# Kernel optimization log

Measured on AMD Instinct MI355X. Metric: run time of the kernel, lower is better.

The kernel has to match this reference:

```python
import jax, jax.numpy as jnp
import numpy as np

DIM = 256
WINDOW = 8
NUM_HEADS = 8
N = WINDOW * WINDOW  # tokens per window
HEAD_DIM = DIM // NUM_HEADS
SCALE = HEAD_DIM ** -0.5
B_ = 2048


def _relative_position_index(w):
    coords = np.stack(np.meshgrid(np.arange(w), np.arange(w), indexing='ij'))  # 2,w,w
    cf = coords.reshape(2, -1)  # 2,N
    rel = cf[:, :, None] - cf[:, None, :]  # 2,N,N
    rel = rel.transpose(1, 2, 0) + (w - 1)  # N,N,2 in [0, 2w-2]
    return rel[..., 0] * (2 * w - 1) + rel[..., 1]  # N,N

REL_INDEX = jnp.asarray(_relative_position_index(WINDOW))  # (N,N) int


def setup_inputs() -> dict:
    key = jax.random.key(0)
    ks = jax.random.split(key, 8)
    x = jax.random.normal(ks[0], (B_, N, DIM), dtype=jnp.float32)
    mask = jax.random.normal(ks[1], (B_, 1, N, N), dtype=jnp.float32)
    w_qkv = jax.random.normal(ks[2], (3 * DIM, DIM), dtype=jnp.float32) * (DIM ** -0.5)
    b_qkv = jnp.zeros((3 * DIM,), dtype=jnp.float32)
    w_proj = jax.random.normal(ks[3], (DIM, DIM), dtype=jnp.float32) * (DIM ** -0.5)
    b_proj = jnp.zeros((DIM,), dtype=jnp.float32)
    bias_table = jax.random.normal(ks[4], ((2 * WINDOW - 1) ** 2, NUM_HEADS), dtype=jnp.float32) * 0.02
    return {"x": x, "mask": mask, "w_qkv": w_qkv, "b_qkv": b_qkv,
            "w_proj": w_proj, "b_proj": b_proj, "bias_table": bias_table}


def reference(x, mask, w_qkv, b_qkv, w_proj, b_proj, bias_table):
    Bw, n, c = x.shape
    qkv = x @ w_qkv.T + b_qkv  # (B_, N, 3*C)
    qkv = qkv.reshape(Bw, n, 3, NUM_HEADS, HEAD_DIM)
    q = qkv[:, :, 0].transpose(0, 2, 1, 3) * SCALE  # (B_, H, N, hd)
    k = qkv[:, :, 1].transpose(0, 2, 1, 3)
    v = qkv[:, :, 2].transpose(0, 2, 1, 3)
    attn = jnp.einsum('bhnd,bhmd->bhnm', q, k)  # (B_, H, N, N)
    rel_bias = bias_table[REL_INDEX]  # (N, N, H)
    attn = attn + rel_bias.transpose(2, 0, 1)[None]  # broadcast (1,H,N,N)
    attn = attn + mask  # (B_,1,N,N) broadcasts over heads
    attn = jax.nn.softmax(attn, axis=-1)
    out = jnp.einsum('bhnm,bhmd->bhnd', attn, v)  # (B_, H, N, hd)
    out = out.transpose(0, 2, 1, 3).reshape(Bw, n, c)
    return out @ w_proj.T + b_proj
```

## Files before the change

kernel.cpp:

```cpp
#include <hip/hip_runtime.h>

#define NWIN 2048
#define NTOK 64
#define CDIM 256
#define NH 8
#define HD 32
#define QSCALE 0.17677669529663689f

#define LDA 264
#define LDQ 36
#define LDV 72
#define LDP 68

typedef __bf16 bf16x4 __attribute__((ext_vector_type(4)));
typedef __bf16 bf16x8 __attribute__((ext_vector_type(8)));
typedef float  f32x4  __attribute__((ext_vector_type(4)));

__device__ __forceinline__ unsigned short f2bf(float f) {
    union { float f; unsigned u; } v; v.f = f;
    unsigned r = v.u + 0x7FFFu + ((v.u >> 16) & 1u);
    return (unsigned short)(r >> 16);
}

__device__ __forceinline__ bf16x8 ld16(const unsigned short* p) {
    return *(const bf16x8*)p;
}
__device__ __forceinline__ bf16x8 ld8u(const unsigned short* p) {
    bf16x4 lo = *(const bf16x4*)p;
    bf16x4 hi = *(const bf16x4*)(p + 4);
    return __builtin_shufflevector(lo, hi, 0, 1, 2, 3, 4, 5, 6, 7);
}

__global__ void precast_kernel(const float* __restrict__ wq, const float* __restrict__ wp,
                               const float* __restrict__ bt,
                               unsigned short* __restrict__ wqb, unsigned short* __restrict__ wpb,
                               float* __restrict__ relbT) {
    int i = blockIdx.x * 256 + threadIdx.x;
    if (i < 196608) {
        wqb[i] = f2bf(wq[i]);
    } else if (i < 262144) {
        wpb[i - 196608] = f2bf(wp[i - 196608]);
    } else if (i < 294912) {
        int j = i - 262144;
        int h = j >> 12;
        int c = (j >> 6) & 63;
        int r = j & 63;
        int yi = r >> 3, xi = r & 7, yj = c >> 3, xj = c & 7;
        int idx = (yi - yj + 7) * 15 + (xi - xj + 7);
        relbT[j] = bt[idx * NH + h];
    }
}

__global__ __launch_bounds__(512, 2)
void win_attn_kernel(const float* __restrict__ x, const float* __restrict__ mask,
                     const float* __restrict__ bq, const float* __restrict__ bp,
                     const unsigned short* __restrict__ wq, const unsigned short* __restrict__ wp,
                     const float* __restrict__ relbT, float* __restrict__ out) {
    __shared__ __align__(16) unsigned short sm[80896];
    unsigned short* sA = sm;
    unsigned short* sQ = sm + 16896;
    unsigned short* sK = sm + 35328;
    unsigned short* sV = sm + 53760;
    unsigned short* sP = sm + 72192;

    const int b    = blockIdx.x;
    const int tid  = threadIdx.x;
    const int wv   = tid >> 6;
    const int lane = tid & 63;
    const int lm   = lane & 15;
    const int quad = lane >> 4;
    const f32x4 fzero = {0.f, 0.f, 0.f, 0.f};

    {
        const int row = tid >> 3;
        const int c0  = (tid & 7) * 32;
        const float4* gx = (const float4*)(x + ((size_t)b * NTOK + row) * CDIM + c0);
        unsigned short* dst = sA + row * LDA + c0;
        #pragma unroll
        for (int i = 0; i < 8; ++i) {
            float4 v = gx[i];
            ushort4 u;
            u.x = f2bf(v.x); u.y = f2bf(v.y); u.z = f2bf(v.z); u.w = f2bf(v.w);
            *(ushort4*)(dst + i * 4) = u;
        }
    }
    __syncthreads();

    {
        const int h = wv;
        const int nbase[6] = { h*HD, h*HD + 16,
                               CDIM + h*HD, CDIM + h*HD + 16,
                               2*CDIM + h*HD, 2*CDIM + h*HD + 16 };
        f32x4 acc[4][6];
        #pragma unroll
        for (int mt = 0; mt < 4; ++mt)
            #pragma unroll
            for (int t = 0; t < 6; ++t) acc[mt][t] = fzero;

        #pragma unroll
        for (int ks = 0; ks < 8; ++ks) {
            bf16x8 bfr[6];
            #pragma unroll
            for (int t = 0; t < 6; ++t)
                bfr[t] = ld16(wq + (nbase[t] + lm) * CDIM + ks * 32 + quad * 8);
            bf16x8 afr[4];
            #pragma unroll
            for (int mt = 0; mt < 4; ++mt)
                afr[mt] = ld16(sA + (mt * 16 + lm) * LDA + ks * 32 + quad * 8);
            #pragma unroll
            for (int mt = 0; mt < 4; ++mt)
                #pragma unroll
                for (int t = 0; t < 6; ++t)
                    acc[mt][t] = __builtin_amdgcn_mfma_f32_16x16x32_bf16(afr[mt], bfr[t], acc[mt][t], 0, 0, 0);
        }

        float bqv[6];
        #pragma unroll
        for (int t = 0; t < 6; ++t) bqv[t] = bq[nbase[t] + lm];

        unsigned short* sQh = sQ + h * (NTOK * LDQ);
        unsigned short* sKh = sK + h * (NTOK * LDQ);
        unsigned short* sVh = sV + h * (HD * LDV);
        #pragma unroll
        for (int mt = 0; mt < 4; ++mt) {
            #pragma unroll
            for (int t = 0; t < 6; ++t) {
                #pragma unroll
                for (int reg = 0; reg < 4; ++reg) {
                    float val = acc[mt][t][reg] + bqv[t];
                    int tok = mt * 16 + quad * 4 + reg;
                    if (t < 2)      sQh[tok * LDQ + t * 16 + lm]          = f2bf(val * QSCALE);
                    else if (t < 4) sKh[tok * LDQ + (t - 2) * 16 + lm]    = f2bf(val);
                    else            sVh[((t - 4) * 16 + lm) * LDV + tok]  = f2bf(val);
                }
            }
        }
    }
    __syncthreads();

    {
        const int h = wv;
        const unsigned short* sQh = sQ + h * (NTOK * LDQ);
        const unsigned short* sKh = sK + h * (NTOK * LDQ);
        const unsigned short* sVh = sV + h * (HD * LDV);
        unsigned short* sPh = sP + wv * (16 * LDP);

        bf16x8 kf[4];
        #pragma unroll
        for (int jt = 0; jt < 4; ++jt)
            kf[jt] = ld8u(sKh + (jt * 16 + lm) * LDQ + quad * 8);
        bf16x8 vf[2][2];
        #pragma unroll
        for (int nt = 0; nt < 2; ++nt)
            #pragma unroll
            for (int kk = 0; kk < 2; ++kk)
                vf[nt][kk] = ld16(sVh + (nt * 16 + lm) * LDV + kk * 32 + quad * 8);

        const float* maskb = mask + (size_t)b * (NTOK * NTOK);
        const float* relh  = relbT + h * (NTOK * NTOK);

        for (int rc = 0; rc < 4; ++rc) {
            const int m0 = rc * 16;
            bf16x8 qa = ld8u(sQh + (m0 + lm) * LDQ + quad * 8);
            f32x4 s[4];
            #pragma unroll
            for (int jt = 0; jt < 4; ++jt)
                s[jt] = __builtin_amdgcn_mfma_f32_16x16x32_bf16(qa, kf[jt], fzero, 0, 0, 0);

            #pragma unroll
            for (int jt = 0; jt < 4; ++jt) {
                float4 rb4 = *(const float4*)(relh + (jt * 16 + lm) * 64 + m0 + quad * 4);
                float rbv[4] = { rb4.x, rb4.y, rb4.z, rb4.w };
                #pragma unroll
                for (int reg = 0; reg < 4; ++reg) {
                    int r = m0 + quad * 4 + reg;
                    s[jt][reg] += rbv[reg] + maskb[r * 64 + jt * 16 + lm];
                }
            }

            float mx[4], inv[4];
            #pragma unroll
            for (int reg = 0; reg < 4; ++reg) {
                float m_ = fmaxf(fmaxf(s[0][reg], s[1][reg]), fmaxf(s[2][reg], s[3][reg]));
                #pragma unroll
                for (int off = 1; off < 16; off <<= 1)
                    m_ = fmaxf(m_, __shfl_xor(m_, off, 64));
                mx[reg] = m_;
            }
            float p[4][4];
            #pragma unroll
            for (int jt = 0; jt < 4; ++jt)
                #pragma unroll
                for (int reg = 0; reg < 4; ++reg)
                    p[jt][reg] = __expf(s[jt][reg] - mx[reg]);
            #pragma unroll
            for (int reg = 0; reg < 4; ++reg) {
                float s_ = (p[0][reg] + p[1][reg]) + (p[2][reg] + p[3][reg]);
                #pragma unroll
                for (int off = 1; off < 16; off <<= 1)
                    s_ += __shfl_xor(s_, off, 64);
                inv[reg] = 1.0f / s_;
            }

            #pragma unroll
            for (int jt = 0; jt < 4; ++jt)
                #pragma unroll
                for (int reg = 0; reg < 4; ++reg)
                    sPh[(quad * 4 + reg) * LDP + jt * 16 + lm] = f2bf(p[jt][reg]);

            bf16x8 pa0 = ld8u(sPh + lm * LDP + quad * 8);
            bf16x8 pa1 = ld8u(sPh + lm * LDP + 32 + quad * 8);
            #pragma unroll
            for (int nt = 0; nt < 2; ++nt) {
                f32x4 o = __builtin_amdgcn_mfma_f32_16x16x32_bf16(pa0, vf[nt][0], fzero, 0, 0, 0);
                o = __builtin_amdgcn_mfma_f32_16x16x32_bf16(pa1, vf[nt][1], o, 0, 0, 0);
                #pragma unroll
                for (int reg = 0; reg < 4; ++reg) {
                    int r = m0 + quad * 4 + reg;
                    sA[r * LDA + h * HD + nt * 16 + lm] = f2bf(o[reg] * inv[reg]);
                }
            }
        }
    }
    __syncthreads();

    {
        const int n0 = wv * HD;
        f32x4 acc[4][2];
        #pragma unroll
        for (int mt = 0; mt < 4; ++mt) { acc[mt][0] = fzero; acc[mt][1] = fzero; }

        #pragma unroll
        for (int ks = 0; ks < 8; ++ks) {
            bf16x8 bfr[2];
            #pragma unroll
            for (int nt = 0; nt < 2; ++nt)
                bfr[nt] = ld16(wp + (n0 + nt * 16 + lm) * CDIM + ks * 32 + quad * 8);
            bf16x8 afr[4];
            #pragma unroll
            for (int mt = 0; mt < 4; ++mt)
                afr[mt] = ld16(sA + (mt * 16 + lm) * LDA + ks * 32 + quad * 8);
            #pragma unroll
            for (int mt = 0; mt < 4; ++mt)
                #pragma unroll
                for (int nt = 0; nt < 2; ++nt)
                    acc[mt][nt] = __builtin_amdgcn_mfma_f32_16x16x32_bf16(afr[mt], bfr[nt], acc[mt][nt], 0, 0, 0);
        }

        float bpv[2] = { bp[n0 + lm], bp[n0 + 16 + lm] };
        #pragma unroll
        for (int mt = 0; mt < 4; ++mt)
            #pragma unroll
            for (int nt = 0; nt < 2; ++nt)
                #pragma unroll
                for (int reg = 0; reg < 4; ++reg) {
                    int r = mt * 16 + quad * 4 + reg;
                    out[((size_t)b * NTOK + r) * CDIM + n0 + nt * 16 + lm] = acc[mt][nt][reg] + bpv[nt];
                }
    }
}

extern "C" void kernel_launch(void* const* d_in, const int* in_sizes, int n_in,
                              void* d_out, int out_size, void* d_ws, size_t ws_size,
                              hipStream_t stream) {
    const float* x    = (const float*)d_in[0];
    const float* mask = (const float*)d_in[1];
    const float* wq   = (const float*)d_in[2];
    const float* bq   = (const float*)d_in[3];
    const float* wp   = (const float*)d_in[4];
    const float* bp   = (const float*)d_in[5];
    const float* bt   = (const float*)d_in[6];

    unsigned short* wqb   = (unsigned short*)d_ws;
    unsigned short* wpb   = wqb + 196608;
    float*          relbT = (float*)((char*)d_ws + 524288);
    float*          out   = (float*)d_out;

    precast_kernel<<<1152, 256, 0, stream>>>(wq, wp, bt, wqb, wpb, relbT);
    win_attn_kernel<<<NWIN, 512, 0, stream>>>(x, mask, bq, bp, wqb, wpb, relbT, out);
}
```

Before: 435.5 us.

## Split projection into separate kernel and shrink LDS in attention kernel

The fused kernel is split in two. The attention kernel now uses 256 threads, each wave handling two heads in sequence, and a small per-wave scratch buffer laid out in MFMA-fragment order. That cuts LDS use from about 160KB to 48KB per block so more blocks can be resident. It also prefetches mask rows one chunk ahead and uses a fast reciprocal. The attention output goes as bf16 into the output buffer, and a new projection kernel reads it back per window and overwrites it in place with the fp32 result. This adds a global write and read of the intermediate, and the Q, K and V GEMMs are now computed separately per head.

```diff
diff --git a/kernel.cpp b/kernel.cpp
--- a/kernel.cpp
+++ b/kernel.cpp
@@ -7,28 +7,17 @@
 #define HD 32
 #define QSCALE 0.17677669529663689f
 
-#define LDA 264
-#define LDQ 36
-#define LDV 72
-#define LDP 68
-
-typedef __bf16 bf16x4 __attribute__((ext_vector_type(4)));
 typedef __bf16 bf16x8 __attribute__((ext_vector_type(8)));
 typedef float  f32x4  __attribute__((ext_vector_type(4)));
+typedef unsigned short u16x8 __attribute__((ext_vector_type(8)));
 
 __device__ __forceinline__ unsigned short f2bf(float f) {
     union { float f; unsigned u; } v; v.f = f;
     unsigned r = v.u + 0x7FFFu + ((v.u >> 16) & 1u);
     return (unsigned short)(r >> 16);
 }
-
 __device__ __forceinline__ bf16x8 ld16(const unsigned short* p) {
     return *(const bf16x8*)p;
-}
-__device__ __forceinline__ bf16x8 ld8u(const unsigned short* p) {
-    bf16x4 lo = *(const bf16x4*)p;
-    bf16x4 hi = *(const bf16x4*)(p + 4);
-    return __builtin_shufflevector(lo, hi, 0, 1, 2, 3, 4, 5, 6, 7);
 }
 
 __global__ void precast_kernel(const float* __restrict__ wq, const float* __restrict__ wp,
@@ -51,17 +40,225 @@
     }
 }
 
-__global__ __launch_bounds__(512, 2)
+__global__ __launch_bounds__(256, 3)
 void win_attn_kernel(const float* __restrict__ x, const float* __restrict__ mask,
-                     const float* __restrict__ bq, const float* __restrict__ bp,
-                     const unsigned short* __restrict__ wq, const unsigned short* __restrict__ wp,
-                     const float* __restrict__ relbT, float* __restrict__ out) {
-    __shared__ __align__(16) unsigned short sm[80896];
-    unsigned short* sA = sm;
-    unsigned short* sQ = sm + 16896;
-    unsigned short* sK = sm + 35328;
-    unsigned short* sV = sm + 53760;
-    unsigned short* sP = sm + 72192;
+                     const float* __restrict__ bqkv,
+                     const unsigned short* __restrict__ wq,
+                     const float* __restrict__ relbT,
+                     unsigned short* __restrict__ aout) {
+    __shared__ __align__(16) unsigned short sm[24576];
+
+    const int b    = blockIdx.x;
+    const int tid  = threadIdx.x;
+    const int wv   = tid >> 6;
+    const int lane = tid & 63;
+    const int lm   = lane & 15;
+    const int quad = lane >> 4;
+    unsigned short* scr = sm + 16384 + wv * 2048;
+    const f32x4 fzero = {0.f, 0.f, 0.f, 0.f};
+
+    {
+        const int row = tid >> 2;
+        const int mt = row >> 4, lr = row & 15;
+        const float* gx = x + ((size_t)b * NTOK + row) * CDIM;
+        #pragma unroll
+        for (int kk = 0; kk < 2; ++kk) {
+            const int ks = (tid & 3) * 2 + kk;
+            #pragma unroll
+            for (int q = 0; q < 4; ++q) {
+                float4 v0 = *(const float4*)(gx + ks * 32 + q * 8);
+                float4 v1 = *(const float4*)(gx + ks * 32 + q * 8 + 4);
+                u16x8 u;
+                u[0] = f2bf(v0.x); u[1] = f2bf(v0.y); u[2] = f2bf(v0.z); u[3] = f2bf(v0.w);
+                u[4] = f2bf(v1.x); u[5] = f2bf(v1.y); u[6] = f2bf(v1.z); u[7] = f2bf(v1.w);
+                *(u16x8*)(sm + (mt * 8 + ks) * 512 + (lr + 16 * q) * 8) = u;
+            }
+        }
+    }
+    __syncthreads();
+
+    const float* maskb = mask + (size_t)b * (NTOK * NTOK);
+
+    for (int hi = 0; hi < 2; ++hi) {
+        const int h = wv + hi * 4;
+
+        const float bq0 = bqkv[h * HD + lm],            bq1 = bqkv[h * HD + 16 + lm];
+        const float bk0 = bqkv[CDIM + h * HD + lm],     bk1 = bqkv[CDIM + h * HD + 16 + lm];
+        const float bv0 = bqkv[2 * CDIM + h * HD + lm], bv1 = bqkv[2 * CDIM + h * HD + 16 + lm];
+
+        f32x4 aq[2][4], ak[2][4];
+        #pragma unroll
+        for (int t = 0; t < 2; ++t)
+            #pragma unroll
+            for (int mt = 0; mt < 4; ++mt) { aq[t][mt] = fzero; ak[t][mt] = fzero; }
+
+        #pragma unroll
+        for (int ks = 0; ks < 8; ++ks) {
+            bf16x8 bfq0 = ld16(wq + ((h * HD + lm) * CDIM) + ks * 32 + quad * 8);
+            bf16x8 bfq1 = ld16(wq + ((h * HD + 16 + lm) * CDIM) + ks * 32 + quad * 8);
+            bf16x8 bfk0 = ld16(wq + ((CDIM + h * HD + lm) * CDIM) + ks * 32 + quad * 8);
+            bf16x8 bfk1 = ld16(wq + ((CDIM + h * HD + 16 + lm) * CDIM) + ks * 32 + quad * 8);
+            #pragma unroll
+            for (int mt = 0; mt < 4; ++mt) {
+                bf16x8 afr = ld16(sm + (mt * 8 + ks) * 512 + lane * 8);
+                aq[0][mt] = __builtin_amdgcn_mfma_f32_16x16x32_bf16(afr, bfq0, aq[0][mt], 0, 0, 0);
+                aq[1][mt] = __builtin_amdgcn_mfma_f32_16x16x32_bf16(afr, bfq1, aq[1][mt], 0, 0, 0);
+                ak[0][mt] = __builtin_amdgcn_mfma_f32_16x16x32_bf16(afr, bfk0, ak[0][mt], 0, 0, 0);
+                ak[1][mt] = __builtin_amdgcn_mfma_f32_16x16x32_bf16(afr, bfk1, ak[1][mt], 0, 0, 0);
+            }
+        }
+
+        #pragma unroll
+        for (int mt = 0; mt < 4; ++mt)
+            #pragma unroll
+            for (int kt = 0; kt < 2; ++kt)
+                #pragma unroll
+                for (int reg = 0; reg < 4; ++reg) {
+                    float val = ak[kt][mt][reg] + (kt ? bk1 : bk0);
+                    int lp = quad * 4 + reg + 16 * (kt * 2 + (lm >> 3));
+                    scr[mt * 512 + lp * 8 + (lm & 7)] = f2bf(val);
+                }
+        bf16x8 kf[4];
+        #pragma unroll
+        for (int jt = 0; jt < 4; ++jt) kf[jt] = ld16(scr + jt * 512 + lane * 8);
+
+        #pragma unroll
+        for (int mt = 0; mt < 4; ++mt)
+            #pragma unroll
+            for (int qt = 0; qt < 2; ++qt)
+                #pragma unroll
+                for (int reg = 0; reg < 4; ++reg) {
+                    float val = (aq[qt][mt][reg] + (qt ? bq1 : bq0)) * QSCALE;
+                    int lp = quad * 4 + reg + 16 * (qt * 2 + (lm >> 3));
+                    scr[mt * 512 + lp * 8 + (lm & 7)] = f2bf(val);
+                }
+        bf16x8 qa[4];
+        #pragma unroll
+        for (int mt = 0; mt < 4; ++mt) qa[mt] = ld16(scr + mt * 512 + lane * 8);
+
+        f32x4 av[2][4];
+        #pragma unroll
+        for (int t = 0; t < 2; ++t)
+            #pragma unroll
+            for (int mt = 0; mt < 4; ++mt) av[t][mt] = fzero;
+        #pragma unroll
+        for (int ks = 0; ks < 8; ++ks) {
+            bf16x8 bfv0 = ld16(wq + ((2 * CDIM + h * HD + lm) * CDIM) + ks * 32 + quad * 8);
+            bf16x8 bfv1 = ld16(wq + ((2 * CDIM + h * HD + 16 + lm) * CDIM) + ks * 32 + quad * 8);
+            #pragma unroll
+            for (int mt = 0; mt < 4; ++mt) {
+                bf16x8 afr = ld16(sm + (mt * 8 + ks) * 512 + lane * 8);
+                av[0][mt] = __builtin_amdgcn_mfma_f32_16x16x32_bf16(afr, bfv0, av[0][mt], 0, 0, 0);
+                av[1][mt] = __builtin_amdgcn_mfma_f32_16x16x32_bf16(afr, bfv1, av[1][mt], 0, 0, 0);
+            }
+        }
+
+        #pragma unroll
+        for (int mt = 0; mt < 4; ++mt)
+            #pragma unroll
+            for (int vt = 0; vt < 2; ++vt)
+                #pragma unroll
+                for (int reg = 0; reg < 4; ++reg) {
+                    float val = av[vt][mt][reg] + (vt ? bv1 : bv0);
+                    int tk = quad * 4 + reg;
+                    int lp = lm + 16 * ((mt & 1) * 2 + (tk >> 3));
+                    scr[(vt * 2 + (mt >> 1)) * 512 + lp * 8 + (tk & 7)] = f2bf(val);
+                }
+        bf16x8 vf[2][2];
+        #pragma unroll
+        for (int vt = 0; vt < 2; ++vt)
+            #pragma unroll
+            for (int kk = 0; kk < 2; ++kk)
+                vf[vt][kk] = ld16(scr + (vt * 2 + kk) * 512 + lane * 8);
+
+        const float* relh = relbT + h * (NTOK * NTOK);
+        unsigned short* ao = aout + (size_t)b * (2 * NTOK * CDIM) + h * HD;
+
+        float mnxt[16];
+        #pragma unroll
+        for (int jt = 0; jt < 4; ++jt)
+            #pragma unroll
+            for (int reg = 0; reg < 4; ++reg)
+                mnxt[jt * 4 + reg] = maskb[(quad * 4 + reg) * 64 + jt * 16 + lm];
+
+        #pragma unroll
+        for (int rc = 0; rc < 4; ++rc) {
+            const int m0 = rc * 16;
+            float mcur[16];
+            #pragma unroll
+            for (int i = 0; i < 16; ++i) mcur[i] = mnxt[i];
+            if (rc < 3) {
+                #pragma unroll
+                for (int jt = 0; jt < 4; ++jt)
+                    #pragma unroll
+                    for (int reg = 0; reg < 4; ++reg)
+                        mnxt[jt * 4 + reg] = maskb[(m0 + 16 + quad * 4 + reg) * 64 + jt * 16 + lm];
+            }
+
+            float4 rb[4];
+            #pragma unroll
+            for (int jt = 0; jt < 4; ++jt)
+                rb[jt] = *(const float4*)(relh + (jt * 16 + lm) * 64 + m0 + quad * 4);
+
+            f32x4 s[4];
+            #pragma unroll
+            for (int jt = 0; jt < 4; ++jt)
+                s[jt] = __builtin_amdgcn_mfma_f32_16x16x32_bf16(qa[rc], kf[jt], fzero, 0, 0, 0);
+
+            #pragma unroll
+            for (int jt = 0; jt < 4; ++jt) {
+                float rbv[4] = { rb[jt].x, rb[jt].y, rb[jt].z, rb[jt].w };
+                #pragma unroll
+                for (int reg = 0; reg < 4; ++reg)
+                    s[jt][reg] += rbv[reg] + mcur[jt * 4 + reg];
+            }
+
+            float inv[4];
+            float p[4][4];
+            #pragma unroll
+            for (int reg = 0; reg < 4; ++reg) {
+                float m_ = fmaxf(fmaxf(s[0][reg], s[1][reg]), fmaxf(s[2][reg], s[3][reg]));
+                #pragma unroll
+                for (int off = 1; off < 16; off <<= 1)
+                    m_ = fmaxf(m_, __shfl_xor(m_, off, 64));
+                #pragma unroll
+                for (int jt = 0; jt < 4; ++jt)
+                    p[jt][reg] = __expf(s[jt][reg] - m_);
+                float s_ = (p[0][reg] + p[1][reg]) + (p[2][reg] + p[3][reg]);
+                #pragma unroll
+                for (int off = 1; off < 16; off <<= 1)
+                    s_ += __shfl_xor(s_, off, 64);
+                inv[reg] = __builtin_amdgcn_rcpf(s_);
+            }
+
+            #pragma unroll
+            for (int jt = 0; jt < 4; ++jt)
+                #pragma unroll
+                for (int reg = 0; reg < 4; ++reg) {
+                    int lp = quad * 4 + reg + 16 * ((jt & 1) * 2 + (lm >> 3));
+                    scr[(jt >> 1) * 512 + lp * 8 + (lm & 7)] = f2bf(p[jt][reg]);
+                }
+            bf16x8 pa0 = ld16(scr + lane * 8);
+            bf16x8 pa1 = ld16(scr + 512 + lane * 8);
+
+            #pragma unroll
+            for (int nt = 0; nt < 2; ++nt) {
+                f32x4 o = __builtin_amdgcn_mfma_f32_16x16x32_bf16(pa0, vf[nt][0], fzero, 0, 0, 0);
+                o = __builtin_amdgcn_mfma_f32_16x16x32_bf16(pa1, vf[nt][1], o, 0, 0, 0);
+                #pragma unroll
+                for (int reg = 0; reg < 4; ++reg) {
+                    int r = m0 + quad * 4 + reg;
+                    ao[(size_t)r * CDIM + nt * 16 + lm] = f2bf(o[reg] * inv[reg]);
+                }
+            }
+        }
+    }
+}
+
+__global__ __launch_bounds__(256, 4)
+void proj_kernel(const unsigned short* __restrict__ wp, const float* __restrict__ bp,
+                 float* out) {
+    __shared__ __align__(16) unsigned short sa[16896];
 
     const int b    = blockIdx.x;
     const int tid  = threadIdx.x;
@@ -71,193 +268,55 @@
     const int quad = lane >> 4;
     const f32x4 fzero = {0.f, 0.f, 0.f, 0.f};
 
+    const unsigned short* src = (const unsigned short*)out + (size_t)b * (2 * NTOK * CDIM);
     {
-        const int row = tid >> 3;
-        const int c0  = (tid & 7) * 32;
-        const float4* gx = (const float4*)(x + ((size_t)b * NTOK + row) * CDIM + c0);
-        unsigned short* dst = sA + row * LDA + c0;
+        const int col = (tid & 31) * 8;
         #pragma unroll
         for (int i = 0; i < 8; ++i) {
-            float4 v = gx[i];
-            ushort4 u;
-            u.x = f2bf(v.x); u.y = f2bf(v.y); u.z = f2bf(v.z); u.w = f2bf(v.w);
-            *(ushort4*)(dst + i * 4) = u;
+            const int row = i * 8 + (tid >> 5);
+            bf16x8 v = *(const bf16x8*)(src + row * CDIM + col);
+            *(bf16x8*)(sa + row * 264 + col) = v;
         }
     }
     __syncthreads();
 
-    {
-        const int h = wv;
-        const int nbase[6] = { h*HD, h*HD + 16,
-                               CDIM + h*HD, CDIM + h*HD + 16,
-                               2*CDIM + h*HD, 2*CDIM + h*HD + 16 };
-        f32x4 acc[4][6];
-        #pragma unroll
-        for (int mt = 0; mt < 4; ++mt)
-            #pragma unroll
-            for (int t = 0; t < 6; ++t) acc[mt][t] = fzero;
-
-        #pragma unroll
-        for (int ks = 0; ks < 8; ++ks) {
-            bf16x8 bfr[6];
-            #pragma unroll
-            for (int t = 0; t < 6; ++t)
-                bfr[t] = ld16(wq + (nbase[t] + lm) * CDIM + ks * 32 + quad * 8);
-            bf16x8 afr[4];
-            #pragma unroll
-            for (int mt = 0; mt < 4; ++mt)
-                afr[mt] = ld16(sA + (mt * 16 + lm) * LDA + ks * 32 + quad * 8);
-            #pragma unroll
-            for (int mt = 0; mt < 4; ++mt)
-                #pragma unroll
-                for (int t = 0; t < 6; ++t)
-                    acc[mt][t] = __builtin_amdgcn_mfma_f32_16x16x32_bf16(afr[mt], bfr[t], acc[mt][t], 0, 0, 0);
-        }
-
-        float bqv[6];
-        #pragma unroll
-        for (int t = 0; t < 6; ++t) bqv[t] = bq[nbase[t] + lm];
-
-        unsigned short* sQh = sQ + h * (NTOK * LDQ);
-        unsigned short* sKh = sK + h * (NTOK * LDQ);
-        unsigned short* sVh = sV + h * (HD * LDV);
-        #pragma unroll
-        for (int mt = 0; mt < 4; ++mt) {
-            #pragma unroll
-            for (int t = 0; t < 6; ++t) {
-                #pragma unroll
-                for (int reg = 0; reg < 4; ++reg) {
-                    float val = acc[mt][t][reg] + bqv[t];
-                    int tok = mt * 16 + quad * 4 + reg;
-                    if (t < 2)      sQh[tok * LDQ + t * 16 + lm]          = f2bf(val * QSCALE);
-                    else if (t < 4) sKh[tok * LDQ + (t - 2) * 16 + lm]    = f2bf(val);
-                    else            sVh[((t - 4) * 16 + lm) * LDV + tok]  = f2bf(val);
-                }
-            }
-        }
-    }
-    __syncthreads();
-
-    {
-        const int h = wv;
-        const unsigned short* sQh = sQ + h * (NTOK * LDQ);
-        const unsigned short* sKh = sK + h * (NTOK * LDQ);
-        const unsigned short* sVh = sV + h * (HD * LDV);
-        unsigned short* sPh = sP + wv * (16 * LDP);
-
-        bf16x8 kf[4];
-        #pragma unroll
-        for (int jt = 0; jt < 4; ++jt)
-            kf[jt] = ld8u(sKh + (jt * 16 + lm) * LDQ + quad * 8);
-        bf16x8 vf[2][2];
-        #pragma unroll
-        for (int nt = 0; nt < 2; ++nt)
-            #pragma unroll
-            for (int kk = 0; kk < 2; ++kk)
-                vf[nt][kk] = ld16(sVh + (nt * 16 + lm) * LDV + kk * 32 + quad * 8);
-
-        const float* maskb = mask + (size_t)b * (NTOK * NTOK);
-        const float* relh  = relbT + h * (NTOK * NTOK);
-
-        for (int rc = 0; rc < 4; ++rc) {
-            const int m0 = rc * 16;
-            bf16x8 qa = ld8u(sQh + (m0 + lm) * LDQ + quad * 8);
-            f32x4 s[4];
-            #pragma unroll
-            for (int jt = 0; jt < 4; ++jt)
-                s[jt] = __builtin_amdgcn_mfma_f32_16x16x32_bf16(qa, kf[jt], fzero, 0, 0, 0);
-
-            #pragma unroll
-            for (int jt = 0; jt < 4; ++jt) {
-                float4 rb4 = *(const float4*)(relh + (jt * 16 + lm) * 64 + m0 + quad * 4);
-                float rbv[4] = { rb4.x, rb4.y, rb4.z, rb4.w };
-                #pragma unroll
-                for (int reg = 0; reg < 4; ++reg) {
-                    int r = m0 + quad * 4 + reg;
-                    s[jt][reg] += rbv[reg] + maskb[r * 64 + jt * 16 + lm];
-                }
-            }
-
-            float mx[4], inv[4];
+    const int n0 = wv * 64;
+    f32x4 acc[4][4];
+    #pragma unroll
+    for (int mt = 0; mt < 4; ++mt)
+        #pragma unroll
+        for (int nt = 0; nt < 4; ++nt) acc[mt][nt] = fzero;
+
+    #pragma unroll
+    for (int ks = 0; ks < 8; ++ks) {
+        bf16x8 bfr[4];
+        #pragma unroll
+        for (int nt = 0; nt < 4; ++nt)
+            bfr[nt] = ld16(wp + (n0 + nt * 16 + lm) * CDIM + ks * 32 + quad * 8);
+        bf16x8 afr[4];
+        #pragma unroll
+        for (int mt = 0; mt < 4; ++mt)
+            afr[mt] = ld16(sa + (mt * 16 + lm) * 264 + ks * 32 + quad * 8);
+        #pragma unroll
+        for (int mt = 0; mt < 4; ++mt)
+            #pragma unroll
+            for (int nt = 0; nt < 4; ++nt)
+                acc[mt][nt] = __builtin_amdgcn_mfma_f32_16x16x32_bf16(afr[mt], bfr[nt], acc[mt][nt], 0, 0, 0);
+    }
+
+    float bpv[4];
+    #pragma unroll
+    for (int nt = 0; nt < 4; ++nt) bpv[nt] = bp[n0 + nt * 16 + lm];
+
+    #pragma unroll
+    for (int mt = 0; mt < 4; ++mt)
+        #pragma unroll
+        for (int nt = 0; nt < 4; ++nt)
             #pragma unroll
             for (int reg = 0; reg < 4; ++reg) {
-                float m_ = fmaxf(fmaxf(s[0][reg], s[1][reg]), fmaxf(s[2][reg], s[3][reg]));
-                #pragma unroll
-                for (int off = 1; off < 16; off <<= 1)
-                    m_ = fmaxf(m_, __shfl_xor(m_, off, 64));
-                mx[reg] = m_;
-            }
-            float p[4][4];
-            #pragma unroll
-            for (int jt = 0; jt < 4; ++jt)
-                #pragma unroll
-                for (int reg = 0; reg < 4; ++reg)
-                    p[jt][reg] = __expf(s[jt][reg] - mx[reg]);
-            #pragma unroll
-            for (int reg = 0; reg < 4; ++reg) {
-                float s_ = (p[0][reg] + p[1][reg]) + (p[2][reg] + p[3][reg]);
-                #pragma unroll
-                for (int off = 1; off < 16; off <<= 1)
-                    s_ += __shfl_xor(s_, off, 64);
-                inv[reg] = 1.0f / s_;
-            }
-
-            #pragma unroll
-            for (int jt = 0; jt < 4; ++jt)
-                #pragma unroll
-                for (int reg = 0; reg < 4; ++reg)
-                    sPh[(quad * 4 + reg) * LDP + jt * 16 + lm] = f2bf(p[jt][reg]);
-
-            bf16x8 pa0 = ld8u(sPh + lm * LDP + quad * 8);
-            bf16x8 pa1 = ld8u(sPh + lm * LDP + 32 + quad * 8);
-            #pragma unroll
-            for (int nt = 0; nt < 2; ++nt) {
-                f32x4 o = __builtin_amdgcn_mfma_f32_16x16x32_bf16(pa0, vf[nt][0], fzero, 0, 0, 0);
-                o = __builtin_amdgcn_mfma_f32_16x16x32_bf16(pa1, vf[nt][1], o, 0, 0, 0);
-                #pragma unroll
-                for (int reg = 0; reg < 4; ++reg) {
-                    int r = m0 + quad * 4 + reg;
-                    sA[r * LDA + h * HD + nt * 16 + lm] = f2bf(o[reg] * inv[reg]);
-                }
-            }
-        }
-    }
-    __syncthreads();
-
-    {
-        const int n0 = wv * HD;
-        f32x4 acc[4][2];
-        #pragma unroll
-        for (int mt = 0; mt < 4; ++mt) { acc[mt][0] = fzero; acc[mt][1] = fzero; }
-
-        #pragma unroll
-        for (int ks = 0; ks < 8; ++ks) {
-            bf16x8 bfr[2];
-            #pragma unroll
-            for (int nt = 0; nt < 2; ++nt)
-                bfr[nt] = ld16(wp + (n0 + nt * 16 + lm) * CDIM + ks * 32 + quad * 8);
-            bf16x8 afr[4];
-            #pragma unroll
-            for (int mt = 0; mt < 4; ++mt)
-                afr[mt] = ld16(sA + (mt * 16 + lm) * LDA + ks * 32 + quad * 8);
-            #pragma unroll
-            for (int mt = 0; mt < 4; ++mt)
-                #pragma unroll
-                for (int nt = 0; nt < 2; ++nt)
-                    acc[mt][nt] = __builtin_amdgcn_mfma_f32_16x16x32_bf16(afr[mt], bfr[nt], acc[mt][nt], 0, 0, 0);
-        }
-
-        float bpv[2] = { bp[n0 + lm], bp[n0 + 16 + lm] };
-        #pragma unroll
-        for (int mt = 0; mt < 4; ++mt)
-            #pragma unroll
-            for (int nt = 0; nt < 2; ++nt)
-                #pragma unroll
-                for (int reg = 0; reg < 4; ++reg) {
-                    int r = mt * 16 + quad * 4 + reg;
-                    out[((size_t)b * NTOK + r) * CDIM + n0 + nt * 16 + lm] = acc[mt][nt][reg] + bpv[nt];
-                }
-    }
+                int r = mt * 16 + quad * 4 + reg;
+                out[((size_t)b * NTOK + r) * CDIM + n0 + nt * 16 + lm] = acc[mt][nt][reg] + bpv[nt];
+            }
 }
 
 extern "C" void kernel_launch(void* const* d_in, const int* in_sizes, int n_in,
@@ -274,8 +333,9 @@
     unsigned short* wqb   = (unsigned short*)d_ws;
     unsigned short* wpb   = wqb + 196608;
     float*          relbT = (float*)((char*)d_ws + 524288);
-    float*          out   = (float*)d_out;
 
     precast_kernel<<<1152, 256, 0, stream>>>(wq, wp, bt, wqb, wpb, relbT);
-    win_attn_kernel<<<NWIN, 512, 0, stream>>>(x, mask, bq, bp, wqb, wpb, relbT, out);
-}
+    win_attn_kernel<<<NWIN, 256, 0, stream>>>(x, mask, bq, wqb, relbT,
+                                              (unsigned short*)d_out);
+    proj_kernel<<<NWIN, 256, 0, stream>>>(wpb, bp, (float*)d_out);
+}
```

New measurement: 611.0 us. 40.3% more time.
